# Optimization experiments

Hardware: AMD Instinct MI355X
Metric: run time of the kernel (lower is better)

The kernel has to match this reference:

```python
import jax, jax.numpy as jnp
import numpy as np

T_DIFF = 1000.0
LN_EPS = 1e-5


def _lin(x, w, b):
    return jnp.matmul(x, w.T) + b


def _ln(x, g, b):
    m = jnp.mean(x, axis=-1, keepdims=True)
    v = jnp.mean((x - m) ** 2, axis=-1, keepdims=True)
    return (x - m) / jnp.sqrt(v + LN_EPS) * g + b


def _pos_lin(x, w, b):
    return jnp.matmul(x, jax.nn.softplus(w).T) + b


def _gamma(t, g_l1_w, g_l1_b, g_l2_w, g_l2_b, g_l3_w, g_l3_b, gamma_0, gamma_1):
    def gtilde(u):
        l1 = _pos_lin(u, g_l1_w, g_l1_b)
        return l1 + _pos_lin(jax.nn.sigmoid(_pos_lin(l1, g_l2_w, g_l2_b)), g_l3_w, g_l3_b)
    g0, g1, gt = gtilde(jnp.zeros_like(t)), gtilde(jnp.ones_like(t)), gtilde(t)
    return gamma_0 + (gamma_1 - gamma_0) * (gt - g0) / (g1 - g0)


def _pair_dist(a):
    # safe pairwise euclidean distances, (B,N,N,1)
    diff = a[:, :, None, :] - a[:, None, :, :]
    d2 = jnp.sum(diff * diff, axis=-1, keepdims=True)
    return diff, jnp.sqrt(jnp.maximum(d2, 1e-12)), d2


def _egc_layer(x, h, x0, p):
    _, d0, _ = _pair_dist(x0)                      # original distances
    diff, dist, d2 = _pair_dist(x)                 # current distances (pre-LN x)
    h = _ln(h, p['lnh_g'], p['lnh_b'])
    x = _ln(x, p['lnx_g'], p['lnx_b'])
    B, N, F = h.shape
    h_i = jnp.broadcast_to(h[:, :, None, :], (B, N, N, F))
    h_j = jnp.broadcast_to(h[:, None, :, :], (B, N, N, F))
    einp = jnp.concatenate([h_i, h_j, d2, d0], axis=-1)  # (B,N,N,2F+2)
    m = jax.nn.silu(_lin(einp, p['edg1_w'], p['edg1_b']))
    m = jax.nn.silu(_lin(m, p['edg2_w'], p['edg2_b']))
    e = jax.nn.sigmoid(_lin(m, p['edgi_w'], p['edgi_b']))
    e = e * (1.0 - jnp.eye(N, dtype=e.dtype)[None, :, :, None])
    m_agg = jnp.sum(e * m, axis=2)                 # sum over j -> (B,N,F)
    hn = jax.nn.silu(_lin(jnp.concatenate([h, m_agg], axis=-1), p['node1_w'], p['node1_b']))
    hn = h + _lin(hn, p['node2_w'], p['node2_b'])
    cw = jax.nn.silu(_lin(einp, p['cor1_w'], p['cor1_b']))
    cw = jax.nn.silu(_lin(cw, p['cor2_w'], p['cor2_b']))
    cw = _lin(cw, p['cor3_w'], p['cor3_b'])        # (B,N,N,1)
    x_next = x + jnp.sum(cw * (diff / (dist + 1.0)), axis=2)
    return x_next, hn


def setup_inputs() -> dict:
    key = jax.random.key(0)
    ks = iter(jax.random.split(key, 64))
    B, N, H, L = 8, 192, 32, 4
    d = {}
    d['xyz_atom_species'] = jax.random.normal(next(ks), (B, N, 4), jnp.float32)
    d['pdf'] = jax.random.normal(next(ks), (B, 3000), jnp.float32)
    d['t'] = jax.random.uniform(next(ks), (B,), jnp.float32) * T_DIFF

    def w(k, shape):
        fan_in = shape[-1]
        return jax.random.normal(k, shape, jnp.float32) / np.sqrt(fan_in)

    d['emb_in_w'] = w(next(ks), (H, 12)); d['emb_in_b'] = jnp.zeros((H,), jnp.float32)
    d['emb_out_w'] = w(next(ks), (1, H)); d['emb_out_b'] = jnp.zeros((1,), jnp.float32)
    d['x_out_w'] = w(next(ks), (3, 3)); d['x_out_b'] = jnp.zeros((3,), jnp.float32)
    d['pdf_w'] = w(next(ks), (10, 3000)); d['pdf_b'] = jnp.zeros((10,), jnp.float32)
    d['g_l1_w'] = w(next(ks), (1, 1)); d['g_l1_b'] = jnp.zeros((1,), jnp.float32)
    d['g_l2_w'] = w(next(ks), (1024, 1)); d['g_l2_b'] = jnp.zeros((1024,), jnp.float32)
    d['g_l3_w'] = w(next(ks), (1, 1024)); d['g_l3_b'] = jnp.zeros((1,), jnp.float32)
    d['gamma_0'] = jnp.array([-5.0], jnp.float32)
    d['gamma_1'] = jnp.array([10.0], jnp.float32)
    d['lnh_g'] = jnp.ones((L, H), jnp.float32); d['lnh_b'] = jnp.zeros((L, H), jnp.float32)
    d['lnx_g'] = jnp.ones((L, 3), jnp.float32); d['lnx_b'] = jnp.zeros((L, 3), jnp.float32)
    d['edg1_w'] = w(next(ks), (L, H, 2 * H + 2)); d['edg1_b'] = jnp.zeros((L, H), jnp.float32)
    d['edg2_w'] = w(next(ks), (L, H, H)); d['edg2_b'] = jnp.zeros((L, H), jnp.float32)
    d['edgi_w'] = w(next(ks), (L, 1, H)); d['edgi_b'] = jnp.zeros((L, 1), jnp.float32)
    d['node1_w'] = w(next(ks), (L, H, 2 * H)); d['node1_b'] = jnp.zeros((L, H), jnp.float32)
    d['node2_w'] = w(next(ks), (L, H, H)); d['node2_b'] = jnp.zeros((L, H), jnp.float32)
    d['cor1_w'] = w(next(ks), (L, H, 2 * H + 2)); d['cor1_b'] = jnp.zeros((L, H), jnp.float32)
    d['cor2_w'] = w(next(ks), (L, H, H)); d['cor2_b'] = jnp.zeros((L, H), jnp.float32)
    d['cor3_w'] = w(next(ks), (L, 1, H)); d['cor3_b'] = jnp.zeros((L, 1), jnp.float32)
    return d


def reference(xyz_atom_species, pdf, t, emb_in_w, emb_in_b, emb_out_w, emb_out_b,
              x_out_w, x_out_b, pdf_w, pdf_b, g_l1_w, g_l1_b, g_l2_w, g_l2_b,
              g_l3_w, g_l3_b, gamma_0, gamma_1, lnh_g, lnh_b, lnx_g, lnx_b,
              edg1_w, edg1_b, edg2_w, edg2_b, edgi_w, edgi_b, node1_w, node1_b,
              node2_w, node2_b, cor1_w, cor1_b, cor2_w, cor2_b, cor3_w, cor3_b):
    B, N, _ = xyz_atom_species.shape
    h = xyz_atom_species[:, :, 3:4]                # (B,N,1)
    x = xyz_atom_species[:, :, :3]
    x0 = x
    tn = (t / T_DIFF)[:, None]                     # (B,1)
    t_emb = _gamma(tn, g_l1_w, g_l1_b, g_l2_w, g_l2_b, g_l3_w, g_l3_b, gamma_0, gamma_1)
    pdf_emb = _lin(pdf, pdf_w, pdf_b)              # (B,10)
    h = jnp.concatenate([
        h,
        jnp.broadcast_to(t_emb[:, None, :], (B, N, 1)),
        jnp.broadcast_to(pdf_emb[:, None, :], (B, N, 10)),
    ], axis=-1)
    h = _lin(h, emb_in_w, emb_in_b)                # (B,N,32)
    for l in range(4):
        p = dict(lnh_g=lnh_g[l], lnh_b=lnh_b[l], lnx_g=lnx_g[l], lnx_b=lnx_b[l],
                 edg1_w=edg1_w[l], edg1_b=edg1_b[l], edg2_w=edg2_w[l], edg2_b=edg2_b[l],
                 edgi_w=edgi_w[l], edgi_b=edgi_b[l], node1_w=node1_w[l], node1_b=node1_b[l],
                 node2_w=node2_w[l], node2_b=node2_b[l], cor1_w=cor1_w[l], cor1_b=cor1_b[l],
                 cor2_w=cor2_w[l], cor2_b=cor2_b[l], cor3_w=cor3_w[l], cor3_b=cor3_b[l])
        x, h = _egc_layer(x, h, x0, p)
    h = _lin(h, emb_out_w, emb_out_b)
    x = _lin(x, x_out_w, x_out_b) - x0
    return jnp.concatenate([x, h], axis=-1)        # (B,N,4)
```

## Files before the change

### kernel.cpp

```cpp
#include <hip/hip_runtime.h>
#include <hip/hip_bf16.h>
#include <math.h>

#define BATCH 8
#define NATOMS 192
#define HF 32

using short8 = __attribute__((ext_vector_type(8))) short;
using f32x4  = __attribute__((ext_vector_type(4))) float;

__device__ __forceinline__ float fast_rcp(float x){ return __builtin_amdgcn_rcpf(x); }
__device__ __forceinline__ float sigmoid_f(float x){ return fast_rcp(1.0f+__expf(-x)); }
__device__ __forceinline__ float silu_f(float x){ return x*fast_rcp(1.0f+__expf(-x)); }
__device__ __forceinline__ float softplus_f(float x){ return fmaxf(x,0.0f)+log1pf(expf(-fabsf(x))); }
__device__ __forceinline__ unsigned short f2bf(float x){
  __hip_bfloat16 h = __float2bfloat16(x);
  return __builtin_bit_cast(unsigned short, h);
}

__device__ __forceinline__ float wave_sum(float v){
  v += __shfl_xor(v, 1);
  v += __shfl_xor(v, 2);
  v += __shfl_xor(v, 4);
  v += __shfl_xor(v, 8);
  v += __shfl_xor(v, 16);
  v += __shfl_xor(v, 32);
  return v;
}

__global__ __launch_bounds__(256) void k_prelude(
    const float* __restrict__ pdf, const float* __restrict__ t,
    const float* __restrict__ pdf_w, const float* __restrict__ pdf_b,
    const float* __restrict__ g1w, const float* __restrict__ g1b,
    const float* __restrict__ g2w, const float* __restrict__ g2b,
    const float* __restrict__ g3w, const float* __restrict__ g3b,
    const float* __restrict__ gamma0, const float* __restrict__ gamma1,
    const float* __restrict__ e2w, const float* __restrict__ c2w,
    unsigned short* __restrict__ e2wb, unsigned short* __restrict__ c2wb,
    float* __restrict__ temb, float* __restrict__ pdfe)
{
  __shared__ float lds[4];
  const int bx = blockIdx.x, tid = threadIdx.x;
  const int wv = tid >> 6, ln = tid & 63;

  if (bx >= 88){
    const int g = (bx - 88)*256 + tid;
    e2wb[g] = f2bf(e2w[g]);
    c2wb[g] = f2bf(c2w[g]);
    return;
  }
  if (bx < 80){
    const int b = bx / 10, o = bx % 10;
    const float* pb = pdf + b*3000;
    const float* wb = pdf_w + o*3000;
    float p = 0.f;
    for (int k = tid; k < 3000; k += 256) p = fmaf(pb[k], wb[k], p);
    p = wave_sum(p);
    if (ln == 0) lds[wv] = p;
    __syncthreads();
    if (tid == 0) pdfe[b*10 + o] = lds[0] + lds[1] + lds[2] + lds[3] + pdf_b[o];
    return;
  }
  const int b = bx - 80;
  const float w1 = softplus_f(g1w[0]);
  const float b1 = g1b[0];
  const float tn = t[b] * (1.0f/1000.0f);
  const float l1_0 = b1;
  const float l1_1 = w1 + b1;
  const float l1_t = fmaf(w1, tn, b1);
  float a0 = 0.f, a1 = 0.f, at = 0.f;
  for (int k = tid; k < 1024; k += 256){
    float w2 = softplus_f(g2w[k]);
    float bb = g2b[k];
    float w3 = softplus_f(g3w[k]);
    a0 += sigmoid_f(fmaf(w2, l1_0, bb)) * w3;
    a1 += sigmoid_f(fmaf(w2, l1_1, bb)) * w3;
    at += sigmoid_f(fmaf(w2, l1_t, bb)) * w3;
  }
  float sums[3]; float vals[3] = {a0, a1, at};
  for (int r = 0; r < 3; ++r){
    float v = wave_sum(vals[r]);
    __syncthreads();
    if (ln == 0) lds[wv] = v;
    __syncthreads();
    sums[r] = lds[0] + lds[1] + lds[2] + lds[3];
  }
  if (tid == 0){
    const float b3 = g3b[0];
    const float g0 = l1_0 + sums[0] + b3;
    const float g1v = l1_1 + sums[1] + b3;
    const float gt = l1_t + sums[2] + b3;
    temb[b] = gamma0[0] + (gamma1[0] - gamma0[0]) * (gt - g0) / (g1v - g0);
  }
}

__global__ __launch_bounds__(256) void k_embed_node(
    const float* __restrict__ xyz, const float* __restrict__ temb,
    const float* __restrict__ pdfe, const float* __restrict__ wi,
    const float* __restrict__ bi,
    const float* __restrict__ lnhg, const float* __restrict__ lnhb,
    const float* __restrict__ e1w, const float* __restrict__ e1b,
    const float* __restrict__ c1w, const float* __restrict__ c1b,
    float* __restrict__ x, float* __restrict__ hln,
    float* __restrict__ ue, float* __restrict__ uc,
    float* __restrict__ vep, float* __restrict__ vcp)
{
  __shared__ float s_h[8][33];
  const int tid = threadIdx.x;
  const int il = tid >> 5, f = tid & 31;
  const int node = blockIdx.x*8 + il;
  const int b = node / NATOMS;

  {
    const float sp = xyz[node*4 + 3];
    const float* w = wi + f*12;
    float a = bi[f];
    a = fmaf(sp, w[0], a);
    a = fmaf(temb[b], w[1], a);
    const float* pe = pdfe + b*10;
#pragma unroll
    for (int p = 0; p < 10; ++p) a = fmaf(pe[p], w[2+p], a);
    s_h[il][f] = a;
  }
  if (f < 3) x[node*3 + f] = xyz[node*4 + f];
  __syncthreads();

  float hl[32];
  float m = 0.f;
#pragma unroll
  for (int k = 0; k < 32; ++k){ hl[k] = s_h[il][k]; m += hl[k]; }
  m *= (1.0f/32.0f);
  float v = 0.f;
#pragma unroll
  for (int k = 0; k < 32; ++k){ float d = hl[k]-m; v = fmaf(d, d, v); }
  float r = rsqrtf(v*(1.0f/32.0f) + 1e-5f);
#pragma unroll
  for (int k = 0; k < 32; ++k) hl[k] = fmaf((hl[k]-m)*r, lnhg[k], lnhb[k]);
  hln[node*32 + f] = hl[f];

  const float* we = e1w + f*66;
  float sv = e1b[f], su = 0.f;
#pragma unroll
  for (int k = 0; k < 32; ++k){ sv = fmaf(hl[k], we[k], sv); su = fmaf(hl[k], we[32+k], su); }
  vep[node*32 + f] = sv;
  ue [node*32 + f] = su;

  const float* wc = c1w + f*66;
  float cv = c1b[f], cu = 0.f;
#pragma unroll
  for (int k = 0; k < 32; ++k){ cv = fmaf(hl[k], wc[k], cv); cu = fmaf(hl[k], wc[32+k], cu); }
  vcp[node*32 + f] = cv;
  uc [node*32 + f] = cu;
}

__global__ __launch_bounds__(384, 2) void k_pair(
    const float* __restrict__ xin, const float* __restrict__ xyz,
    const float* __restrict__ hln, const float* __restrict__ ue,
    const float* __restrict__ uc, const float* __restrict__ vep,
    const float* __restrict__ vcp,
    const float* __restrict__ e1w, const float* __restrict__ c1w,
    const unsigned short* __restrict__ e2wb, const unsigned short* __restrict__ c2wb,
    const float* __restrict__ e2b, const float* __restrict__ eiw,
    const float* __restrict__ eib,
    const float* __restrict__ c2b, const float* __restrict__ c3w,
    const float* __restrict__ c3b,
    const float* __restrict__ n1w, const float* __restrict__ n1b,
    const float* __restrict__ n2w, const float* __restrict__ n2b,
    const float* __restrict__ lnxg, const float* __restrict__ lnxb,
    const float* __restrict__ lnhg_n, const float* __restrict__ lnhb_n,
    const float* __restrict__ e1w_n, const float* __restrict__ e1b_n,
    const float* __restrict__ c1w_n, const float* __restrict__ c1b_n,
    float* __restrict__ hln_n, float* __restrict__ ue_n,
    float* __restrict__ uc_n, float* __restrict__ vep_n,
    float* __restrict__ vcp_n, float* __restrict__ xout,
    const float* __restrict__ how, const float* __restrict__ hob,
    const float* __restrict__ xow, const float* __restrict__ xob,
    float* __restrict__ dout, const int lastl)
{
  __shared__ float s_geo[NATOMS][6];
  __shared__ unsigned short s_m1[NATOMS][40];
  __shared__ unsigned short s_c1[NATOMS][40];
  __shared__ unsigned short s_we[32][40];
  __shared__ unsigned short s_wc[32][40];
  __shared__ float s_pm[3][32];
  __shared__ float s_pxc[3][3];

  const int i = blockIdx.x, b = blockIdx.y;
  const int tid = threadIdx.x;
  const int base = b * NATOMS;
  const int node = base + i;
  const int g = tid >> 7;
  const int t = tid & 127;
  const int lane = t & 63;
  const int isCor = t >> 6;
  const int n = lane & 15, quad = lane >> 4;

  if (tid < NATOMS){
    const int j = tid;
    const float* xi_p = xin + node*3;
    const float* xj_p = xin + (base + j)*3;
    const float dfx = xi_p[0] - xj_p[0], dfy = xi_p[1] - xj_p[1], dfz = xi_p[2] - xj_p[2];
    const float d2 = dfx*dfx + dfy*dfy + dfz*dfz;
    const float dist = sqrtf(fmaxf(d2, 1e-12f));
    const float* x0i = xyz + node*4;
    const float* x0j = xyz + (base + j)*4;
    const float q0 = x0i[0]-x0j[0], q1 = x0i[1]-x0j[1], q2 = x0i[2]-x0j[2];
    const float d0 = sqrtf(fmaxf(q0*q0 + q1*q1 + q2*q2, 1e-12f));
    s_geo[j][0] = dfx; s_geo[j][1] = dfy; s_geo[j][2] = dfz;
    s_geo[j][3] = d2;  s_geo[j][4] = d0;  s_geo[j][5] = dist;
  } else {
    const int u = tid - NATOMS;
    const short8* es = (const short8*)e2wb;
    const short8* cs = (const short8*)c2wb;
    if (u < 128){
      const int f = u >> 2, kq = u & 3;
      *(short8*)&s_we[f][kq*8] = es[u];
    }
    if (u >= 64){
      const int c = u - 64;
      const int f = c >> 2, kq = c & 3;
      *(short8*)&s_wc[f][kq*8] = cs[c];
    }
  }
  __syncthreads();

  {
    const int kk = t & 31, jg = t >> 5;
    const float vpe = vep[node*32 + kk];
    const float vpc = vcp[node*32 + kk];
    const float we64 = e1w[kk*66 + 64], we65 = e1w[kk*66 + 65];
    const float wc64 = c1w[kk*66 + 64], wc65 = c1w[kk*66 + 65];
#pragma unroll
    for (int jj = jg; jj < 64; jj += 4){
      const int row = g*64 + jj;
      const float d2 = s_geo[row][3], d0 = s_geo[row][4];
      const float uev = ue[(size_t)(base + row)*32 + kk];
      const float m1 = silu_f(fmaf(d2, we64, fmaf(d0, we65, vpe + uev)));
      s_m1[row][kk] = f2bf(m1);
      const float ucv = uc[(size_t)(base + row)*32 + kk];
      const float c1 = silu_f(fmaf(d2, wc64, fmaf(d0, wc65, vpc + ucv)));
      s_c1[row][kk] = f2bf(c1);
    }
  }
  __syncthreads();

  if (isCor == 0){
    const float eb0 = e2b[n], eb1 = e2b[16 + n];
    const float ew0 = eiw[n], ew1 = eiw[16 + n];
    const float ebias = eib[0];
    float ma0 = 0.f, ma1 = 0.f;
    short8 b0 = *(const short8*)&s_we[n][quad*8];
    short8 b1 = *(const short8*)&s_we[16 + n][quad*8];
#pragma unroll
    for (int jt = 0; jt < 4; ++jt){
      short8 a = *(const short8*)&s_m1[g*64 + jt*16 + n][quad*8];
      f32x4 z = {0.f, 0.f, 0.f, 0.f};
      f32x4 acc0 = __builtin_amdgcn_mfma_f32_16x16x32_bf16(a, b0, z, 0, 0, 0);
      f32x4 acc1 = __builtin_amdgcn_mfma_f32_16x16x32_bf16(a, b1, z, 0, 0, 0);
      float m20[4], m21[4], gg[4];
#pragma unroll
      for (int r = 0; r < 4; ++r){
        m20[r] = silu_f(acc0[r] + eb0);
        m21[r] = silu_f(acc1[r] + eb1);
        gg[r] = m20[r]*ew0 + m21[r]*ew1;
      }
#pragma unroll
      for (int r = 0; r < 4; ++r){
        gg[r] += __shfl_xor(gg[r], 1);
        gg[r] += __shfl_xor(gg[r], 2);
        gg[r] += __shfl_xor(gg[r], 4);
        gg[r] += __shfl_xor(gg[r], 8);
      }
#pragma unroll
      for (int r = 0; r < 4; ++r){
        const int jglob = g*64 + jt*16 + quad*4 + r;
        const float e = (jglob == i) ? 0.0f : sigmoid_f(gg[r] + ebias);
        ma0 = fmaf(e, m20[r], ma0);
        ma1 = fmaf(e, m21[r], ma1);
      }
    }
    ma0 += __shfl_xor(ma0, 16); ma0 += __shfl_xor(ma0, 32);
    ma1 += __shfl_xor(ma1, 16); ma1 += __shfl_xor(ma1, 32);
    if (lane < 16){
      s_pm[g][lane] = ma0;
      s_pm[g][16 + lane] = ma1;
    }
  } else {
    const float cb0 = c2b[n], cb1 = c2b[16 + n];
    const float cw0 = c3w[n], cw1 = c3w[16 + n];
    const float cbias = c3b[0];
    float px = 0.f, py = 0.f, pz = 0.f;
    short8 b0 = *(const short8*)&s_wc[n][quad*8];
    short8 b1 = *(const short8*)&s_wc[16 + n][quad*8];
#pragma unroll
    for (int jt = 0; jt < 4; ++jt){
      short8 a = *(const short8*)&s_c1[g*64 + jt*16 + n][quad*8];
      f32x4 z = {0.f, 0.f, 0.f, 0.f};
      f32x4 acc0 = __builtin_amdgcn_mfma_f32_16x16x32_bf16(a, b0, z, 0, 0, 0);
      f32x4 acc1 = __builtin_amdgcn_mfma_f32_16x16x32_bf16(a, b1, z, 0, 0, 0);
      float gg[4];
#pragma unroll
      for (int r = 0; r < 4; ++r){
        gg[r] = silu_f(acc0[r] + cb0)*cw0 + silu_f(acc1[r] + cb1)*cw1;
      }
#pragma unroll
      for (int r = 0; r < 4; ++r){
        gg[r] += __shfl_xor(gg[r], 1);
        gg[r] += __shfl_xor(gg[r], 2);
        gg[r] += __shfl_xor(gg[r], 4);
        gg[r] += __shfl_xor(gg[r], 8);
      }
#pragma unroll
      for (int r = 0; r < 4; ++r){
        const int row = g*64 + jt*16 + quad*4 + r;
        const float s = (gg[r] + cbias) * fast_rcp(s_geo[row][5] + 1.0f);
        px = fmaf(s, s_geo[row][0], px);
        py = fmaf(s, s_geo[row][1], py);
        pz = fmaf(s, s_geo[row][2], pz);
      }
    }
    px += __shfl_xor(px, 16); px += __shfl_xor(px, 32);
    py += __shfl_xor(py, 16); py += __shfl_xor(py, 32);
    pz += __shfl_xor(pz, 16); pz += __shfl_xor(pz, 32);
    if (lane == 0){ s_pxc[g][0] = px; s_pxc[g][1] = py; s_pxc[g][2] = pz; }
  }
  __syncthreads();
  if (tid >= 64) return;

  const int f = tid & 31;
  const float mgf = s_pm[0][f] + s_pm[1][f] + s_pm[2][f];
  const float hlf = hln[node*32 + f];

  float a = n1b[f];
  const float* w1 = n1w + f*64;
#pragma unroll
  for (int k = 0; k < 32; ++k) a = fmaf(__shfl(hlf, k, 64), w1[k], a);
#pragma unroll
  for (int k = 0; k < 32; ++k) a = fmaf(__shfl(mgf, k, 64), w1[32 + k], a);
  const float n1v = silu_f(a);
  float o = n2b[f];
  const float* w2 = n2w + f*32;
#pragma unroll
  for (int k = 0; k < 32; ++k) o = fmaf(__shfl(n1v, k, 64), w2[k], o);
  const float ho = hlf + o;

  float xn0, xn1, xn2;
  {
    const float* xr = xin + node*3;
    const float x0 = xr[0], x1 = xr[1], x2 = xr[2];
    const float mx = (x0 + x1 + x2) * (1.0f/3.0f);
    const float v0 = x0-mx, v1 = x1-mx, v2 = x2-mx;
    const float r = rsqrtf((v0*v0 + v1*v1 + v2*v2)*(1.0f/3.0f) + 1e-5f);
    xn0 = fmaf(v0*r, lnxg[0], lnxb[0]) + s_pxc[0][0] + s_pxc[1][0] + s_pxc[2][0];
    xn1 = fmaf(v1*r, lnxg[1], lnxb[1]) + s_pxc[0][1] + s_pxc[1][1] + s_pxc[2][1];
    xn2 = fmaf(v2*r, lnxg[2], lnxb[2]) + s_pxc[0][2] + s_pxc[1][2] + s_pxc[2][2];
  }

  if (!lastl){
    if (tid == 0){
      float* xo = xout + node*3;
      xo[0] = xn0; xo[1] = xn1; xo[2] = xn2;
    }
    float s = ho;
    s += __shfl_xor(s, 1); s += __shfl_xor(s, 2); s += __shfl_xor(s, 4);
    s += __shfl_xor(s, 8); s += __shfl_xor(s, 16);
    const float m = s * (1.0f/32.0f);
    const float d = ho - m;
    float vv = d*d;
    vv += __shfl_xor(vv, 1); vv += __shfl_xor(vv, 2); vv += __shfl_xor(vv, 4);
    vv += __shfl_xor(vv, 8); vv += __shfl_xor(vv, 16);
    const float r = rsqrtf(vv*(1.0f/32.0f) + 1e-5f);
    const float hl = fmaf(d*r, lnhg_n[f], lnhb_n[f]);
    if (tid < 32) hln_n[node*32 + f] = hl;

    const float* we = e1w_n + f*66;
    const float* wc = c1w_n + f*66;
    float sv = e1b_n[f], su = 0.f, cv = c1b_n[f], cu = 0.f;
#pragma unroll
    for (int k = 0; k < 32; ++k){
      const float tkk = __shfl(hl, k, 64);
      sv = fmaf(tkk, we[k], sv);
      su = fmaf(tkk, we[32 + k], su);
      cv = fmaf(tkk, wc[k], cv);
      cu = fmaf(tkk, wc[32 + k], cu);
    }
    if (tid < 32){
      vep_n[node*32 + f] = sv;
      ue_n [node*32 + f] = su;
      vcp_n[node*32 + f] = cv;
      uc_n [node*32 + f] = cu;
    }
  } else {
    float hh = how[f] * ho;
    hh += __shfl_xor(hh, 1); hh += __shfl_xor(hh, 2); hh += __shfl_xor(hh, 4);
    hh += __shfl_xor(hh, 8); hh += __shfl_xor(hh, 16);
    if (tid == 0) dout[node*4 + 3] = hh + hob[0];
    if (tid < 3){
      const int c = tid;
      float oo = xob[c];
      oo = fmaf(xn0, xow[c*3 + 0], oo);
      oo = fmaf(xn1, xow[c*3 + 1], oo);
      oo = fmaf(xn2, xow[c*3 + 2], oo);
      dout[node*4 + c] = oo - xyz[node*4 + c];
    }
  }
}

extern "C" void kernel_launch(void* const* d_in, const int* in_sizes, int n_in,
                              void* d_out, int out_size, void* d_ws, size_t ws_size,
                              hipStream_t stream)
{
  const float* xyz      = (const float*)d_in[0];
  const float* pdf      = (const float*)d_in[1];
  const float* t        = (const float*)d_in[2];
  const float* emb_in_w = (const float*)d_in[3];
  const float* emb_in_b = (const float*)d_in[4];
  const float* emb_out_w= (const float*)d_in[5];
  const float* emb_out_b= (const float*)d_in[6];
  const float* x_out_w  = (const float*)d_in[7];
  const float* x_out_b  = (const float*)d_in[8];
  const float* pdf_w    = (const float*)d_in[9];
  const float* pdf_b    = (const float*)d_in[10];
  const float* g1w      = (const float*)d_in[11];
  const float* g1b      = (const float*)d_in[12];
  const float* g2w      = (const float*)d_in[13];
  const float* g2b      = (const float*)d_in[14];
  const float* g3w      = (const float*)d_in[15];
  const float* g3b      = (const float*)d_in[16];
  const float* gamma0   = (const float*)d_in[17];
  const float* gamma1   = (const float*)d_in[18];
  const float* lnhg     = (const float*)d_in[19];
  const float* lnhb     = (const float*)d_in[20];
  const float* lnxg     = (const float*)d_in[21];
  const float* lnxb     = (const float*)d_in[22];
  const float* e1w      = (const float*)d_in[23];
  const float* e1b      = (const float*)d_in[24];
  const float* e2w      = (const float*)d_in[25];
  const float* e2b      = (const float*)d_in[26];
  const float* eiw      = (const float*)d_in[27];
  const float* eib      = (const float*)d_in[28];
  const float* n1w      = (const float*)d_in[29];
  const float* n1b      = (const float*)d_in[30];
  const float* n2w      = (const float*)d_in[31];
  const float* n2b      = (const float*)d_in[32];
  const float* c1w      = (const float*)d_in[33];
  const float* c1b      = (const float*)d_in[34];
  const float* c2w      = (const float*)d_in[35];
  const float* c2b      = (const float*)d_in[36];
  const float* c3w      = (const float*)d_in[37];
  const float* c3b      = (const float*)d_in[38];

  const int NTOT = BATCH*NATOMS;
  float* ws   = (float*)d_ws;
  float* temb = ws;
  float* pdfe = ws + 8;
  unsigned short* e2wb = (unsigned short*)(ws + 96);
  unsigned short* c2wb = e2wb + 4096;
  float* p0   = ws + 96 + 4096;
  float* xbA  = p0;                float* xbB  = xbA + NTOT*3;
  float* hlnA = xbB  + NTOT*3;     float* hlnB = hlnA + NTOT*32;
  float* ueA  = hlnB + NTOT*32;    float* ueB  = ueA  + NTOT*32;
  float* ucA  = ueB  + NTOT*32;    float* ucB  = ucA  + NTOT*32;
  float* vepA = ucB  + NTOT*32;    float* vepB = vepA + NTOT*32;
  float* vcpA = vepB + NTOT*32;    float* vcpB = vcpA + NTOT*32;

  float* xb[2]  = {xbA,  xbB};
  float* hlnP[2]= {hlnA, hlnB};
  float* ueP[2] = {ueA,  ueB};
  float* ucP[2] = {ucA,  ucB};
  float* vepP[2]= {vepA, vepB};
  float* vcpP[2]= {vcpA, vcpB};

  k_prelude<<<104, 256, 0, stream>>>(pdf, t, pdf_w, pdf_b,
      g1w, g1b, g2w, g2b, g3w, g3b, gamma0, gamma1,
      e2w, c2w, e2wb, c2wb, temb, pdfe);
  k_embed_node<<<NTOT/8, 256, 0, stream>>>(
      xyz, temb, pdfe, emb_in_w, emb_in_b,
      lnhg, lnhb, e1w, e1b, c1w, c1b,
      xbA, hlnA, ueA, ucA, vepA, vcpA);

  for (int l = 0; l < 4; ++l){
    const int p = l & 1;
    const int nl = (l < 3) ? (l + 1) : 3;
    k_pair<<<dim3(NATOMS, BATCH), 384, 0, stream>>>(
        xb[p], xyz, hlnP[p], ueP[p], ucP[p], vepP[p], vcpP[p],
        e1w + l*2112, c1w + l*2112,
        e2wb + l*1024, c2wb + l*1024,
        e2b + l*32, eiw + l*32, eib + l,
        c2b + l*32, c3w + l*32, c3b + l,
        n1w + l*2048, n1b + l*32, n2w + l*1024, n2b + l*32,
        lnxg + l*3, lnxb + l*3,
        lnhg + nl*32, lnhb + nl*32,
        e1w + nl*2112, e1b + nl*32, c1w + nl*2112, c1b + nl*32,
        hlnP[1-p], ueP[1-p], ucP[1-p], vepP[1-p], vcpP[1-p], xb[1-p],
        emb_out_w, emb_out_b, x_out_w, x_out_b,
        (float*)d_out, (l == 3) ? 1 : 0);
  }
}
```

Before: 275.4 us.

## Prefetch ue/uc rows as float4 and split tail projections across two waves

Each thread now loads a full 32-float ue or uc row with vectorized float4 loads at kernel start, so the global latency overlaps the geometry setup. Per-node first-layer constants go through a shared s_multi buffer, and each thread writes packed bf16 pairs. The pairwise distance is recomputed from d2 instead of being stored, and the next-layer edge and coordinate projections are split between two waves instead of one. In exchange the prologue uses more registers (32 floats per thread), and there is a shared buffer overlap to watch: s_multi rows 0-2 hold vep and the e1w columns until the second barrier and are then overwritten by partial sums.

New measurement: 314.4 us. 14.2% more time.

```diff
diff --git a/kernel.cpp b/kernel.cpp
--- a/kernel.cpp
+++ b/kernel.cpp
@@ -177,23 +177,23 @@
     const float* __restrict__ xow, const float* __restrict__ xob,
     float* __restrict__ dout, const int lastl)
 {
-  __shared__ float s_geo[NATOMS][6];
+  __shared__ float s_geo[NATOMS][5];
   __shared__ unsigned short s_m1[NATOMS][40];
   __shared__ unsigned short s_c1[NATOMS][40];
   __shared__ unsigned short s_we[32][40];
   __shared__ unsigned short s_wc[32][40];
-  __shared__ float s_pm[3][32];
-  __shared__ float s_pxc[3][3];
+  __shared__ float s_multi[6][32];
 
   const int i = blockIdx.x, b = blockIdx.y;
   const int tid = threadIdx.x;
   const int base = b * NATOMS;
   const int node = base + i;
-  const int g = tid >> 7;
-  const int t = tid & 127;
-  const int lane = t & 63;
-  const int isCor = t >> 6;
-  const int n = lane & 15, quad = lane >> 4;
+
+  const int rowp = tid >> 1, sel = tid & 1;
+  const float4* srcRow = (const float4*)((sel ? uc : ue) + (size_t)(base + rowp)*32);
+  float4 u4[8];
+#pragma unroll
+  for (int q = 0; q < 8; ++q) u4[q] = srcRow[q];
 
   if (tid < NATOMS){
     const int j = tid;
@@ -201,134 +201,159 @@
     const float* xj_p = xin + (base + j)*3;
     const float dfx = xi_p[0] - xj_p[0], dfy = xi_p[1] - xj_p[1], dfz = xi_p[2] - xj_p[2];
     const float d2 = dfx*dfx + dfy*dfy + dfz*dfz;
-    const float dist = sqrtf(fmaxf(d2, 1e-12f));
     const float* x0i = xyz + node*4;
     const float* x0j = xyz + (base + j)*4;
     const float q0 = x0i[0]-x0j[0], q1 = x0i[1]-x0j[1], q2 = x0i[2]-x0j[2];
     const float d0 = sqrtf(fmaxf(q0*q0 + q1*q1 + q2*q2, 1e-12f));
     s_geo[j][0] = dfx; s_geo[j][1] = dfy; s_geo[j][2] = dfz;
-    s_geo[j][3] = d2;  s_geo[j][4] = d0;  s_geo[j][5] = dist;
+    s_geo[j][3] = d2;  s_geo[j][4] = d0;
   } else {
-    const int u = tid - NATOMS;
+    const int u2 = tid - NATOMS;
+    const int r6 = u2 >> 5, f = u2 & 31;
+    float v;
+    if      (r6 == 0) v = vep[node*32 + f];
+    else if (r6 == 1) v = e1w[f*66 + 64];
+    else if (r6 == 2) v = e1w[f*66 + 65];
+    else if (r6 == 3) v = vcp[node*32 + f];
+    else if (r6 == 4) v = c1w[f*66 + 64];
+    else              v = c1w[f*66 + 65];
+    s_multi[r6][f] = v;
     const short8* es = (const short8*)e2wb;
     const short8* cs = (const short8*)c2wb;
-    if (u < 128){
-      const int f = u >> 2, kq = u & 3;
-      *(short8*)&s_we[f][kq*8] = es[u];
-    }
-    if (u >= 64){
-      const int c = u - 64;
-      const int f = c >> 2, kq = c & 3;
-      *(short8*)&s_wc[f][kq*8] = cs[c];
-    }
+    if (u2 < 128){ const int ff = u2 >> 2, kq = u2 & 3; *(short8*)&s_we[ff][kq*8] = es[u2]; }
+    if (u2 >= 64){ const int c = u2 - 64; const int ff = c >> 2, kq = c & 3; *(short8*)&s_wc[ff][kq*8] = cs[c]; }
   }
   __syncthreads();
 
   {
-    const int kk = t & 31, jg = t >> 5;
-    const float vpe = vep[node*32 + kk];
-    const float vpc = vcp[node*32 + kk];
-    const float we64 = e1w[kk*66 + 64], we65 = e1w[kk*66 + 65];
-    const float wc64 = c1w[kk*66 + 64], wc65 = c1w[kk*66 + 65];
-#pragma unroll
-    for (int jj = jg; jj < 64; jj += 4){
-      const int row = g*64 + jj;
-      const float d2 = s_geo[row][3], d0 = s_geo[row][4];
-      const float uev = ue[(size_t)(base + row)*32 + kk];
-      const float m1 = silu_f(fmaf(d2, we64, fmaf(d0, we65, vpe + uev)));
-      s_m1[row][kk] = f2bf(m1);
-      const float ucv = uc[(size_t)(base + row)*32 + kk];
-      const float c1 = silu_f(fmaf(d2, wc64, fmaf(d0, wc65, vpc + ucv)));
-      s_c1[row][kk] = f2bf(c1);
+    const float d2r = s_geo[rowp][3], d0r = s_geo[rowp][4];
+    const float* vp  = s_multi[sel*3 + 0];
+    const float* w64 = s_multi[sel*3 + 1];
+    const float* w65 = s_multi[sel*3 + 2];
+    unsigned int* dst = (unsigned int*)(sel ? &s_c1[rowp][0] : &s_m1[rowp][0]);
+#pragma unroll
+    for (int q = 0; q < 8; ++q){
+      const float vv[4] = {u4[q].x, u4[q].y, u4[q].z, u4[q].w};
+#pragma unroll
+      for (int hh = 0; hh < 2; ++hh){
+        unsigned short lo, hi;
+        {
+          const int f = q*4 + hh*2;
+          float a = vp[f] + vv[hh*2];
+          a = fmaf(d2r, w64[f], fmaf(d0r, w65[f], a));
+          lo = f2bf(silu_f(a));
+        }
+        {
+          const int f = q*4 + hh*2 + 1;
+          float a = vp[f] + vv[hh*2 + 1];
+          a = fmaf(d2r, w64[f], fmaf(d0r, w65[f], a));
+          hi = f2bf(silu_f(a));
+        }
+        dst[q*2 + hh] = (unsigned int)lo | ((unsigned int)hi << 16);
+      }
     }
   }
   __syncthreads();
 
-  if (isCor == 0){
-    const float eb0 = e2b[n], eb1 = e2b[16 + n];
-    const float ew0 = eiw[n], ew1 = eiw[16 + n];
-    const float ebias = eib[0];
-    float ma0 = 0.f, ma1 = 0.f;
-    short8 b0 = *(const short8*)&s_we[n][quad*8];
-    short8 b1 = *(const short8*)&s_we[16 + n][quad*8];
-#pragma unroll
-    for (int jt = 0; jt < 4; ++jt){
-      short8 a = *(const short8*)&s_m1[g*64 + jt*16 + n][quad*8];
-      f32x4 z = {0.f, 0.f, 0.f, 0.f};
-      f32x4 acc0 = __builtin_amdgcn_mfma_f32_16x16x32_bf16(a, b0, z, 0, 0, 0);
-      f32x4 acc1 = __builtin_amdgcn_mfma_f32_16x16x32_bf16(a, b1, z, 0, 0, 0);
-      float m20[4], m21[4], gg[4];
-#pragma unroll
-      for (int r = 0; r < 4; ++r){
-        m20[r] = silu_f(acc0[r] + eb0);
-        m21[r] = silu_f(acc1[r] + eb1);
-        gg[r] = m20[r]*ew0 + m21[r]*ew1;
+  {
+    const int g = tid >> 7;
+    const int t = tid & 127;
+    const int lane = t & 63;
+    const int isCor = t >> 6;
+    const int n = lane & 15, quad = lane >> 4;
+
+    if (isCor == 0){
+      const float eb0 = e2b[n], eb1 = e2b[16 + n];
+      const float ew0 = eiw[n], ew1 = eiw[16 + n];
+      const float ebias = eib[0];
+      float ma0 = 0.f, ma1 = 0.f;
+      short8 b0 = *(const short8*)&s_we[n][quad*8];
+      short8 b1 = *(const short8*)&s_we[16 + n][quad*8];
+#pragma unroll
+      for (int jt = 0; jt < 4; ++jt){
+        short8 a = *(const short8*)&s_m1[g*64 + jt*16 + n][quad*8];
+        f32x4 z = {0.f, 0.f, 0.f, 0.f};
+        f32x4 acc0 = __builtin_amdgcn_mfma_f32_16x16x32_bf16(a, b0, z, 0, 0, 0);
+        f32x4 acc1 = __builtin_amdgcn_mfma_f32_16x16x32_bf16(a, b1, z, 0, 0, 0);
+        float m20[4], m21[4], gg[4];
+#pragma unroll
+        for (int r = 0; r < 4; ++r){
+          m20[r] = silu_f(acc0[r] + eb0);
+          m21[r] = silu_f(acc1[r] + eb1);
+          gg[r] = m20[r]*ew0 + m21[r]*ew1;
+        }
+#pragma unroll
+        for (int r = 0; r < 4; ++r){
+          gg[r] += __shfl_xor(gg[r], 1);
+          gg[r] += __shfl_xor(gg[r], 2);
+          gg[r] += __shfl_xor(gg[r], 4);
+          gg[r] += __shfl_xor(gg[r], 8);
+        }
+#pragma unroll
+        for (int r = 0; r < 4; ++r){
+          const int jglob = g*64 + jt*16 + quad*4 + r;
+          const float e = (jglob == i) ? 0.0f : sigmoid_f(gg[r] + ebias);
+          ma0 = fmaf(e, m20[r], ma0);
+          ma1 = fmaf(e, m21[r], ma1);
+        }
       }
-#pragma unroll
-      for (int r = 0; r < 4; ++r){
-        gg[r] += __shfl_xor(gg[r], 1);
-        gg[r] += __shfl_xor(gg[r], 2);
-        gg[r] += __shfl_xor(gg[r], 4);
-        gg[r] += __shfl_xor(gg[r], 8);
+      ma0 += __shfl_xor(ma0, 16); ma0 += __shfl_xor(ma0, 32);
+      ma1 += __shfl_xor(ma1, 16); ma1 += __shfl_xor(ma1, 32);
+      if (lane < 16){
+        s_multi[g][lane] = ma0;
+        s_multi[g][16 + lane] = ma1;
       }
-#pragma unroll
-      for (int r = 0; r < 4; ++r){
-        const int jglob = g*64 + jt*16 + quad*4 + r;
-        const float e = (jglob == i) ? 0.0f : sigmoid_f(gg[r] + ebias);
-        ma0 = fmaf(e, m20[r], ma0);
-        ma1 = fmaf(e, m21[r], ma1);
+    } else {
+      const float cb0 = c2b[n], cb1 = c2b[16 + n];
+      const float cw0 = c3w[n], cw1 = c3w[16 + n];
+      const float cbias = c3b[0];
+      float px = 0.f, py = 0.f, pz = 0.f;
+      short8 b0 = *(const short8*)&s_wc[n][quad*8];
+      short8 b1 = *(const short8*)&s_wc[16 + n][quad*8];
+#pragma unroll
+      for (int jt = 0; jt < 4; ++jt){
+        short8 a = *(const short8*)&s_c1[g*64 + jt*16 + n][quad*8];
+        f32x4 z = {0.f, 0.f, 0.f, 0.f};
+        f32x4 acc0 = __builtin_amdgcn_mfma_f32_16x16x32_bf16(a, b0, z, 0, 0, 0);
+        f32x4 acc1 = __builtin_amdgcn_mfma_f32_16x16x32_bf16(a, b1, z, 0, 0, 0);
+        float gg[4];
+#pragma unroll
+        for (int r = 0; r < 4; ++r){
+          gg[r] = silu_f(acc0[r] + cb0)*cw0 + silu_f(acc1[r] + cb1)*cw1;
+        }
+#pragma unroll
+        for (int r = 0; r < 4; ++r){
+          gg[r] += __shfl_xor(gg[r], 1);
+          gg[r] += __shfl_xor(gg[r], 2);
+          gg[r] += __shfl_xor(gg[r], 4);
+          gg[r] += __shfl_xor(gg[r], 8);
+        }
+#pragma unroll
+        for (int r = 0; r < 4; ++r){
+          const int row = g*64 + jt*16 + quad*4 + r;
+          const float dist = sqrtf(fmaxf(s_geo[row][3], 1e-12f));
+          const float s = (gg[r] + cbias) * fast_rcp(dist + 1.0f);
+          px = fmaf(s, s_geo[row][0], px);
+          py = fmaf(s, s_geo[row][1], py);
+          pz = fmaf(s, s_geo[row][2], pz);
+        }
       }
-    }
-    ma0 += __shfl_xor(ma0, 16); ma0 += __shfl_xor(ma0, 32);
-    ma1 += __shfl_xor(ma1, 16); ma1 += __shfl_xor(ma1, 32);
-    if (lane < 16){
-      s_pm[g][lane] = ma0;
-      s_pm[g][16 + lane] = ma1;
-    }
-  } else {
-    const float cb0 = c2b[n], cb1 = c2b[16 + n];
-    const float cw0 = c3w[n], cw1 = c3w[16 + n];
-    const float cbias = c3b[0];
-    float px = 0.f, py = 0.f, pz = 0.f;
-    short8 b0 = *(const short8*)&s_wc[n][quad*8];
-    short8 b1 = *(const short8*)&s_wc[16 + n][quad*8];
-#pragma unroll
-    for (int jt = 0; jt < 4; ++jt){
-      short8 a = *(const short8*)&s_c1[g*64 + jt*16 + n][quad*8];
-      f32x4 z = {0.f, 0.f, 0.f, 0.f};
-      f32x4 acc0 = __builtin_amdgcn_mfma_f32_16x16x32_bf16(a, b0, z, 0, 0, 0);
-      f32x4 acc1 = __builtin_amdgcn_mfma_f32_16x16x32_bf16(a, b1, z, 0, 0, 0);
-      float gg[4];
-#pragma unroll
-      for (int r = 0; r < 4; ++r){
-        gg[r] = silu_f(acc0[r] + cb0)*cw0 + silu_f(acc1[r] + cb1)*cw1;
+      px += __shfl_xor(px, 16); px += __shfl_xor(px, 32);
+      py += __shfl_xor(py, 16); py += __shfl_xor(py, 32);
+      pz += __shfl_xor(pz, 16); pz += __shfl_xor(pz, 32);
+      if (lane == 0){
+        s_multi[3][g*3 + 0] = px;
+        s_multi[3][g*3 + 1] = py;
+        s_multi[3][g*3 + 2] = pz;
       }
-#pragma unroll
-      for (int r = 0; r < 4; ++r){
-        gg[r] += __shfl_xor(gg[r], 1);
-        gg[r] += __shfl_xor(gg[r], 2);
-        gg[r] += __shfl_xor(gg[r], 4);
-        gg[r] += __shfl_xor(gg[r], 8);
-      }
-#pragma unroll
-      for (int r = 0; r < 4; ++r){
-        const int row = g*64 + jt*16 + quad*4 + r;
-        const float s = (gg[r] + cbias) * fast_rcp(s_geo[row][5] + 1.0f);
-        px = fmaf(s, s_geo[row][0], px);
-        py = fmaf(s, s_geo[row][1], py);
-        pz = fmaf(s, s_geo[row][2], pz);
-      }
-    }
-    px += __shfl_xor(px, 16); px += __shfl_xor(px, 32);
-    py += __shfl_xor(py, 16); py += __shfl_xor(py, 32);
-    pz += __shfl_xor(pz, 16); pz += __shfl_xor(pz, 32);
-    if (lane == 0){ s_pxc[g][0] = px; s_pxc[g][1] = py; s_pxc[g][2] = pz; }
+    }
   }
   __syncthreads();
-  if (tid >= 64) return;
+  if (tid >= 128) return;
 
   const int f = tid & 31;
-  const float mgf = s_pm[0][f] + s_pm[1][f] + s_pm[2][f];
+  const int pw = tid >> 6;
+  const float mgf = s_multi[0][f] + s_multi[1][f] + s_multi[2][f];
   const float hlf = hln[node*32 + f];
 
   float a = n1b[f];
@@ -344,53 +369,16 @@
   for (int k = 0; k < 32; ++k) o = fmaf(__shfl(n1v, k, 64), w2[k], o);
   const float ho = hlf + o;
 
-  float xn0, xn1, xn2;
-  {
+  if (lastl){
+    if (tid >= 64) return;
     const float* xr = xin + node*3;
     const float x0 = xr[0], x1 = xr[1], x2 = xr[2];
     const float mx = (x0 + x1 + x2) * (1.0f/3.0f);
     const float v0 = x0-mx, v1 = x1-mx, v2 = x2-mx;
     const float r = rsqrtf((v0*v0 + v1*v1 + v2*v2)*(1.0f/3.0f) + 1e-5f);
-    xn0 = fmaf(v0*r, lnxg[0], lnxb[0]) + s_pxc[0][0] + s_pxc[1][0] + s_pxc[2][0];
-    xn1 = fmaf(v1*r, lnxg[1], lnxb[1]) + s_pxc[0][1] + s_pxc[1][1] + s_pxc[2][1];
-    xn2 = fmaf(v2*r, lnxg[2], lnxb[2]) + s_pxc[0][2] + s_pxc[1][2] + s_pxc[2][2];
-  }
-
-  if (!lastl){
-    if (tid == 0){
-      float* xo = xout + node*3;
-      xo[0] = xn0; xo[1] = xn1; xo[2] = xn2;
-    }
-    float s = ho;
-    s += __shfl_xor(s, 1); s += __shfl_xor(s, 2); s += __shfl_xor(s, 4);
-    s += __shfl_xor(s, 8); s += __shfl_xor(s, 16);
-    const float m = s * (1.0f/32.0f);
-    const float d = ho - m;
-    float vv = d*d;
-    vv += __shfl_xor(vv, 1); vv += __shfl_xor(vv, 2); vv += __shfl_xor(vv, 4);
-    vv += __shfl_xor(vv, 8); vv += __shfl_xor(vv, 16);
-    const float r = rsqrtf(vv*(1.0f/32.0f) + 1e-5f);
-    const float hl = fmaf(d*r, lnhg_n[f], lnhb_n[f]);
-    if (tid < 32) hln_n[node*32 + f] = hl;
-
-    const float* we = e1w_n + f*66;
-    const float* wc = c1w_n + f*66;
-    float sv = e1b_n[f], su = 0.f, cv = c1b_n[f], cu = 0.f;
-#pragma unroll
-    for (int k = 0; k < 32; ++k){
-      const float tkk = __shfl(hl, k, 64);
-      sv = fmaf(tkk, we[k], sv);
-      su = fmaf(tkk, we[32 + k], su);
-      cv = fmaf(tkk, wc[k], cv);
-      cu = fmaf(tkk, wc[32 + k], cu);
-    }
-    if (tid < 32){
-      vep_n[node*32 + f] = sv;
-      ue_n [node*32 + f] = su;
-      vcp_n[node*32 + f] = cv;
-      uc_n [node*32 + f] = cu;
-    }
-  } else {
+    const float xn0 = fmaf(v0*r, lnxg[0], lnxb[0]) + s_multi[3][0] + s_multi[3][3] + s_multi[3][6];
+    const float xn1 = fmaf(v1*r, lnxg[1], lnxb[1]) + s_multi[3][1] + s_multi[3][4] + s_multi[3][7];
+    const float xn2 = fmaf(v2*r, lnxg[2], lnxb[2]) + s_multi[3][2] + s_multi[3][5] + s_multi[3][8];
     float hh = how[f] * ho;
     hh += __shfl_xor(hh, 1); hh += __shfl_xor(hh, 2); hh += __shfl_xor(hh, 4);
     hh += __shfl_xor(hh, 8); hh += __shfl_xor(hh, 16);
@@ -402,6 +390,58 @@
       oo = fmaf(xn1, xow[c*3 + 1], oo);
       oo = fmaf(xn2, xow[c*3 + 2], oo);
       dout[node*4 + c] = oo - xyz[node*4 + c];
+    }
+    return;
+  }
+
+  float s = ho;
+  s += __shfl_xor(s, 1); s += __shfl_xor(s, 2); s += __shfl_xor(s, 4);
+  s += __shfl_xor(s, 8); s += __shfl_xor(s, 16);
+  const float m = s * (1.0f/32.0f);
+  const float d = ho - m;
+  float vv = d*d;
+  vv += __shfl_xor(vv, 1); vv += __shfl_xor(vv, 2); vv += __shfl_xor(vv, 4);
+  vv += __shfl_xor(vv, 8); vv += __shfl_xor(vv, 16);
+  const float r = rsqrtf(vv*(1.0f/32.0f) + 1e-5f);
+  const float hl = fmaf(d*r, lnhg_n[f], lnhb_n[f]);
+
+  if (pw == 0){
+    const float* we = e1w_n + f*66;
+    float sv = e1b_n[f], su = 0.f;
+#pragma unroll
+    for (int k = 0; k < 32; ++k){
+      const float tkk = __shfl(hl, k, 64);
+      sv = fmaf(tkk, we[k], sv);
+      su = fmaf(tkk, we[32 + k], su);
+    }
+    if (tid < 32){
+      hln_n[node*32 + f] = hl;
+      vep_n[node*32 + f] = sv;
+      ue_n [node*32 + f] = su;
+    }
+  } else {
+    const float* wc = c1w_n + f*66;
+    float cv = c1b_n[f], cu = 0.f;
+#pragma unroll
+    for (int k = 0; k < 32; ++k){
+      const float tkk = __shfl(hl, k, 64);
+      cv = fmaf(tkk, wc[k], cv);
+      cu = fmaf(tkk, wc[32 + k], cu);
+    }
+    if ((tid & 63) < 32){
+      vcp_n[node*32 + f] = cv;
+      uc_n [node*32 + f] = cu;
+    }
+    if ((tid & 63) == 0){
+      const float* xr = xin + node*3;
+      const float x0 = xr[0], x1 = xr[1], x2 = xr[2];
+      const float mx = (x0 + x1 + x2) * (1.0f/3.0f);
+      const float v0 = x0-mx, v1 = x1-mx, v2 = x2-mx;
+      const float rr = rsqrtf((v0*v0 + v1*v1 + v2*v2)*(1.0f/3.0f) + 1e-5f);
+      float* xo = xout + node*3;
+      xo[0] = fmaf(v0*rr, lnxg[0], lnxb[0]) + s_multi[3][0] + s_multi[3][3] + s_multi[3][6];
+      xo[1] = fmaf(v1*rr, lnxg[1], lnxb[1]) + s_multi[3][1] + s_multi[3][4] + s_multi[3][7];
+      xo[2] = fmaf(v2*rr, lnxg[2], lnxb[2]) + s_multi[3][2] + s_multi[3][5] + s_multi[3][8];
     }
   }
 }
```

## Fuse geometry and first-layer edge activation into one phase, drop a barrier

Applied to the files above, without the earlier changes.

Merges the geometry setup and the first edge/coord layer activation into a single phase. Each thread now owns one (row, branch) pair, loads its 32-wide ue/uc row with vector loads, and writes packed bf16 rows to shared memory. This removes one __syncthreads and the strided scalar global reads, and the distance is now recomputed from d2 in the coord branch instead of being kept in shared memory. It also raises the launch-bounds occupancy hint from 2 to 4 blocks, which may force register spills given the 32-float u4 array and the per-thread weight loads.

Result: slower. 301.6 us (+9.5%).

```diff
diff --git a/kernel.cpp b/kernel.cpp
--- a/kernel.cpp
+++ b/kernel.cpp
@@ -153,7 +153,7 @@
   uc [node*32 + f] = cu;
 }
 
-__global__ __launch_bounds__(384, 2) void k_pair(
+__global__ __launch_bounds__(384, 4) void k_pair(
     const float* __restrict__ xin, const float* __restrict__ xyz,
     const float* __restrict__ hln, const float* __restrict__ ue,
     const float* __restrict__ uc, const float* __restrict__ vep,
@@ -177,7 +177,7 @@
     const float* __restrict__ xow, const float* __restrict__ xob,
     float* __restrict__ dout, const int lastl)
 {
-  __shared__ float s_geo[NATOMS][6];
+  __shared__ float s_geo[NATOMS][4];
   __shared__ unsigned short s_m1[NATOMS][40];
   __shared__ unsigned short s_c1[NATOMS][40];
   __shared__ unsigned short s_we[32][40];
@@ -189,140 +189,167 @@
   const int tid = threadIdx.x;
   const int base = b * NATOMS;
   const int node = base + i;
-  const int g = tid >> 7;
-  const int t = tid & 127;
-  const int lane = t & 63;
-  const int isCor = t >> 6;
-  const int n = lane & 15, quad = lane >> 4;
-
-  if (tid < NATOMS){
-    const int j = tid;
+
+  {
+    const int sel = (tid >= NATOMS) ? 1 : 0;
+    const int row = tid - sel*NATOMS;
+
+    const float4* srcRow = (const float4*)((sel ? uc : ue) + (size_t)(base + row)*32);
+    float4 u4[8];
+#pragma unroll
+    for (int q = 0; q < 8; ++q) u4[q] = srcRow[q];
+
+    if (tid < 128){
+      const int f = tid >> 2, kq = tid & 3;
+      *(short8*)&s_we[f][kq*8] = ((const short8*)e2wb)[tid];
+    } else if (tid < 256){
+      const int c = tid - 128;
+      const int f = c >> 2, kq = c & 3;
+      *(short8*)&s_wc[f][kq*8] = ((const short8*)c2wb)[c];
+    }
+
     const float* xi_p = xin + node*3;
-    const float* xj_p = xin + (base + j)*3;
+    const float* xj_p = xin + (base + row)*3;
     const float dfx = xi_p[0] - xj_p[0], dfy = xi_p[1] - xj_p[1], dfz = xi_p[2] - xj_p[2];
     const float d2 = dfx*dfx + dfy*dfy + dfz*dfz;
-    const float dist = sqrtf(fmaxf(d2, 1e-12f));
     const float* x0i = xyz + node*4;
-    const float* x0j = xyz + (base + j)*4;
+    const float* x0j = xyz + (base + row)*4;
     const float q0 = x0i[0]-x0j[0], q1 = x0i[1]-x0j[1], q2 = x0i[2]-x0j[2];
     const float d0 = sqrtf(fmaxf(q0*q0 + q1*q1 + q2*q2, 1e-12f));
-    s_geo[j][0] = dfx; s_geo[j][1] = dfy; s_geo[j][2] = dfz;
-    s_geo[j][3] = d2;  s_geo[j][4] = d0;  s_geo[j][5] = dist;
-  } else {
-    const int u = tid - NATOMS;
-    const short8* es = (const short8*)e2wb;
-    const short8* cs = (const short8*)c2wb;
-    if (u < 128){
-      const int f = u >> 2, kq = u & 3;
-      *(short8*)&s_we[f][kq*8] = es[u];
-    }
-    if (u >= 64){
-      const int c = u - 64;
-      const int f = c >> 2, kq = c & 3;
-      *(short8*)&s_wc[f][kq*8] = cs[c];
+    if (tid < NATOMS){
+      s_geo[row][0] = dfx; s_geo[row][1] = dfy; s_geo[row][2] = dfz;
+      s_geo[row][3] = d2;
+    }
+
+    const float* vp  = (sel ? vcp : vep) + node*32;
+    const float* wp  = sel ? c1w : e1w;
+    unsigned short* dst = sel ? &s_c1[row][0] : &s_m1[row][0];
+#pragma unroll
+    for (int half = 0; half < 2; ++half){
+      uint4 wword;
+      unsigned int wtmp[4];
+#pragma unroll
+      for (int p = 0; p < 4; ++p){
+        const int q = half*4 + p;
+        const float vv[4] = {u4[q].x, u4[q].y, u4[q].z, u4[q].w};
+        unsigned int wlo, whi;
+        {
+          const int f = q*4 + 0;
+          float a = silu_f(fmaf(d2, wp[f*66+64], fmaf(d0, wp[f*66+65], vp[f] + vv[0])));
+          const int f2 = q*4 + 1;
+          float a2 = silu_f(fmaf(d2, wp[f2*66+64], fmaf(d0, wp[f2*66+65], vp[f2] + vv[1])));
+          wlo = (unsigned int)f2bf(a) | ((unsigned int)f2bf(a2) << 16);
+        }
+        {
+          const int f = q*4 + 2;
+          float a = silu_f(fmaf(d2, wp[f*66+64], fmaf(d0, wp[f*66+65], vp[f] + vv[2])));
+          const int f2 = q*4 + 3;
+          float a2 = silu_f(fmaf(d2, wp[f2*66+64], fmaf(d0, wp[f2*66+65], vp[f2] + vv[3])));
+          whi = (unsigned int)f2bf(a) | ((unsigned int)f2bf(a2) << 16);
+        }
+        wtmp[p*2 % 4]     = wlo;
+        wtmp[(p*2 % 4)+1] = whi;
+        if (p == 1){
+          wword.x = wtmp[0]; wword.y = wtmp[1]; wword.z = wtmp[2]; wword.w = wtmp[3];
+          *(uint4*)&dst[half*16] = wword;
+        }
+        if (p == 3){
+          wword.x = wtmp[0]; wword.y = wtmp[1]; wword.z = wtmp[2]; wword.w = wtmp[3];
+          *(uint4*)&dst[half*16 + 8] = wword;
+        }
+      }
     }
   }
   __syncthreads();
 
   {
-    const int kk = t & 31, jg = t >> 5;
-    const float vpe = vep[node*32 + kk];
-    const float vpc = vcp[node*32 + kk];
-    const float we64 = e1w[kk*66 + 64], we65 = e1w[kk*66 + 65];
-    const float wc64 = c1w[kk*66 + 64], wc65 = c1w[kk*66 + 65];
-#pragma unroll
-    for (int jj = jg; jj < 64; jj += 4){
-      const int row = g*64 + jj;
-      const float d2 = s_geo[row][3], d0 = s_geo[row][4];
-      const float uev = ue[(size_t)(base + row)*32 + kk];
-      const float m1 = silu_f(fmaf(d2, we64, fmaf(d0, we65, vpe + uev)));
-      s_m1[row][kk] = f2bf(m1);
-      const float ucv = uc[(size_t)(base + row)*32 + kk];
-      const float c1 = silu_f(fmaf(d2, wc64, fmaf(d0, wc65, vpc + ucv)));
-      s_c1[row][kk] = f2bf(c1);
-    }
-  }
-  __syncthreads();
-
-  if (isCor == 0){
-    const float eb0 = e2b[n], eb1 = e2b[16 + n];
-    const float ew0 = eiw[n], ew1 = eiw[16 + n];
-    const float ebias = eib[0];
-    float ma0 = 0.f, ma1 = 0.f;
-    short8 b0 = *(const short8*)&s_we[n][quad*8];
-    short8 b1 = *(const short8*)&s_we[16 + n][quad*8];
-#pragma unroll
-    for (int jt = 0; jt < 4; ++jt){
-      short8 a = *(const short8*)&s_m1[g*64 + jt*16 + n][quad*8];
-      f32x4 z = {0.f, 0.f, 0.f, 0.f};
-      f32x4 acc0 = __builtin_amdgcn_mfma_f32_16x16x32_bf16(a, b0, z, 0, 0, 0);
-      f32x4 acc1 = __builtin_amdgcn_mfma_f32_16x16x32_bf16(a, b1, z, 0, 0, 0);
-      float m20[4], m21[4], gg[4];
-#pragma unroll
-      for (int r = 0; r < 4; ++r){
-        m20[r] = silu_f(acc0[r] + eb0);
-        m21[r] = silu_f(acc1[r] + eb1);
-        gg[r] = m20[r]*ew0 + m21[r]*ew1;
+    const int g = tid >> 7;
+    const int t = tid & 127;
+    const int lane = t & 63;
+    const int isCor = t >> 6;
+    const int n = lane & 15, quad = lane >> 4;
+
+    if (isCor == 0){
+      const float eb0 = e2b[n], eb1 = e2b[16 + n];
+      const float ew0 = eiw[n], ew1 = eiw[16 + n];
+      const float ebias = eib[0];
+      float ma0 = 0.f, ma1 = 0.f;
+      short8 b0 = *(const short8*)&s_we[n][quad*8];
+      short8 b1 = *(const short8*)&s_we[16 + n][quad*8];
+#pragma unroll
+      for (int jt = 0; jt < 4; ++jt){
+        short8 a = *(const short8*)&s_m1[g*64 + jt*16 + n][quad*8];
+        f32x4 z = {0.f, 0.f, 0.f, 0.f};
+        f32x4 acc0 = __builtin_amdgcn_mfma_f32_16x16x32_bf16(a, b0, z, 0, 0, 0);
+        f32x4 acc1 = __builtin_amdgcn_mfma_f32_16x16x32_bf16(a, b1, z, 0, 0, 0);
+        float m20[4], m21[4], gg[4];
+#pragma unroll
+        for (int r = 0; r < 4; ++r){
+          m20[r] = silu_f(acc0[r] + eb0);
+          m21[r] = silu_f(acc1[r] + eb1);
+          gg[r] = m20[r]*ew0 + m21[r]*ew1;
+        }
+#pragma unroll
+        for (int r = 0; r < 4; ++r){
+          gg[r] += __shfl_xor(gg[r], 1);
+          gg[r] += __shfl_xor(gg[r], 2);
+          gg[r] += __shfl_xor(gg[r], 4);
+          gg[r] += __shfl_xor(gg[r], 8);
+        }
+#pragma unroll
+        for (int r = 0; r < 4; ++r){
+          const int jglob = g*64 + jt*16 + quad*4 + r;
+          const float e = (jglob == i) ? 0.0f : sigmoid_f(gg[r] + ebias);
+          ma0 = fmaf(e, m20[r], ma0);
+          ma1 = fmaf(e, m21[r], ma1);
+        }
       }
-#pragma unroll
-      for (int r = 0; r < 4; ++r){
-        gg[r] += __shfl_xor(gg[r], 1);
-        gg[r] += __shfl_xor(gg[r], 2);
-        gg[r] += __shfl_xor(gg[r], 4);
-        gg[r] += __shfl_xor(gg[r], 8);
+      ma0 += __shfl_xor(ma0, 16); ma0 += __shfl_xor(ma0, 32);
+      ma1 += __shfl_xor(ma1, 16); ma1 += __shfl_xor(ma1, 32);
+      if (lane < 16){
+        s_pm[g][lane] = ma0;
+        s_pm[g][16 + lane] = ma1;
       }
-#pragma unroll
-      for (int r = 0; r < 4; ++r){
-        const int jglob = g*64 + jt*16 + quad*4 + r;
-        const float e = (jglob == i) ? 0.0f : sigmoid_f(gg[r] + ebias);
-        ma0 = fmaf(e, m20[r], ma0);
-        ma1 = fmaf(e, m21[r], ma1);
+    } else {
+      const float cb0 = c2b[n], cb1 = c2b[16 + n];
+      const float cw0 = c3w[n], cw1 = c3w[16 + n];
+      const float cbias = c3b[0];
+      float px = 0.f, py = 0.f, pz = 0.f;
+      short8 b0 = *(const short8*)&s_wc[n][quad*8];
+      short8 b1 = *(const short8*)&s_wc[16 + n][quad*8];
+#pragma unroll
+      for (int jt = 0; jt < 4; ++jt){
+        short8 a = *(const short8*)&s_c1[g*64 + jt*16 + n][quad*8];
+        f32x4 z = {0.f, 0.f, 0.f, 0.f};
+        f32x4 acc0 = __builtin_amdgcn_mfma_f32_16x16x32_bf16(a, b0, z, 0, 0, 0);
+        f32x4 acc1 = __builtin_amdgcn_mfma_f32_16x16x32_bf16(a, b1, z, 0, 0, 0);
+        float gg[4];
+#pragma unroll
+        for (int r = 0; r < 4; ++r){
+          gg[r] = silu_f(acc0[r] + cb0)*cw0 + silu_f(acc1[r] + cb1)*cw1;
+        }
+#pragma unroll
+        for (int r = 0; r < 4; ++r){
+          gg[r] += __shfl_xor(gg[r], 1);
+          gg[r] += __shfl_xor(gg[r], 2);
+          gg[r] += __shfl_xor(gg[r], 4);
+          gg[r] += __shfl_xor(gg[r], 8);
+        }
+#pragma unroll
+        for (int r = 0; r < 4; ++r){
+          const int row = g*64 + jt*16 + quad*4 + r;
+          const float dist = sqrtf(fmaxf(s_geo[row][3], 1e-12f));
+          const float s = (gg[r] + cbias) * fast_rcp(dist + 1.0f);
+          px = fmaf(s, s_geo[row][0], px);
+          py = fmaf(s, s_geo[row][1], py);
+          pz = fmaf(s, s_geo[row][2], pz);
+        }
       }
-    }
-    ma0 += __shfl_xor(ma0, 16); ma0 += __shfl_xor(ma0, 32);
-    ma1 += __shfl_xor(ma1, 16); ma1 += __shfl_xor(ma1, 32);
-    if (lane < 16){
-      s_pm[g][lane] = ma0;
-      s_pm[g][16 + lane] = ma1;
-    }
-  } else {
-    const float cb0 = c2b[n], cb1 = c2b[16 + n];
-    const float cw0 = c3w[n], cw1 = c3w[16 + n];
-    const float cbias = c3b[0];
-    float px = 0.f, py = 0.f, pz = 0.f;
-    short8 b0 = *(const short8*)&s_wc[n][quad*8];
-    short8 b1 = *(const short8*)&s_wc[16 + n][quad*8];
-#pragma unroll
-    for (int jt = 0; jt < 4; ++jt){
-      short8 a = *(const short8*)&s_c1[g*64 + jt*16 + n][quad*8];
-      f32x4 z = {0.f, 0.f, 0.f, 0.f};
-      f32x4 acc0 = __builtin_amdgcn_mfma_f32_16x16x32_bf16(a, b0, z, 0, 0, 0);
-      f32x4 acc1 = __builtin_amdgcn_mfma_f32_16x16x32_bf16(a, b1, z, 0, 0, 0);
-      float gg[4];
-#pragma unroll
-      for (int r = 0; r < 4; ++r){
-        gg[r] = silu_f(acc0[r] + cb0)*cw0 + silu_f(acc1[r] + cb1)*cw1;
-      }
-#pragma unroll
-      for (int r = 0; r < 4; ++r){
-        gg[r] += __shfl_xor(gg[r], 1);
-        gg[r] += __shfl_xor(gg[r], 2);
-        gg[r] += __shfl_xor(gg[r], 4);
-        gg[r] += __shfl_xor(gg[r], 8);
-      }
-#pragma unroll
-      for (int r = 0; r < 4; ++r){
-        const int row = g*64 + jt*16 + quad*4 + r;
-        const float s = (gg[r] + cbias) * fast_rcp(s_geo[row][5] + 1.0f);
-        px = fmaf(s, s_geo[row][0], px);
-        py = fmaf(s, s_geo[row][1], py);
-        pz = fmaf(s, s_geo[row][2], pz);
-      }
-    }
-    px += __shfl_xor(px, 16); px += __shfl_xor(px, 32);
-    py += __shfl_xor(py, 16); py += __shfl_xor(py, 32);
-    pz += __shfl_xor(pz, 16); pz += __shfl_xor(pz, 32);
-    if (lane == 0){ s_pxc[g][0] = px; s_pxc[g][1] = py; s_pxc[g][2] = pz; }
+      px += __shfl_xor(px, 16); px += __shfl_xor(px, 32);
+      py += __shfl_xor(py, 16); py += __shfl_xor(py, 32);
+      pz += __shfl_xor(pz, 16); pz += __shfl_xor(pz, 32);
+      if (lane == 0){ s_pxc[g][0] = px; s_pxc[g][1] = py; s_pxc[g][2] = pz; }
+    }
   }
   __syncthreads();
   if (tid >= 64) return;
```
